# Kernel optimization log

Hardware: AMD Instinct MI355X
Metric: run time of the kernel (lower is better)

## Reference

```python
import jax, jax.numpy as jnp
import numpy as np

N = 262144
BN_EPS = 1e-5


def gcn_conv(x, edge_index, edge_weight, W, b):
    """PyG GCNConv: symmetric norm with added self-loops (fill value 1).
    out[i] = sum_e d^{-1/2}[src] * w_e * d^{-1/2}[dst] * (x[src] @ W) + b
    """
    src, dst = edge_index[0], edge_index[1]
    loops = jnp.arange(N)
    src2 = jnp.concatenate([src, loops])
    dst2 = jnp.concatenate([dst, loops])
    ew2 = jnp.concatenate([edge_weight, jnp.ones((N,), edge_weight.dtype)])
    deg = jax.ops.segment_sum(ew2, dst2, num_segments=N)  # [N]
    dinv = jnp.where(deg > 0, jax.lax.rsqrt(deg), 0.0)
    norm = dinv[src2] * ew2 * dinv[dst2]  # [E+N]
    h = x @ W  # [N, out_c] tiny GEMM
    msg = h[src2] * norm[:, None]  # gather + scale, [E+N, out_c]
    out = jax.ops.segment_sum(msg, dst2, num_segments=N)  # scatter-add
    return out + b


def bn_eval(x, gamma, beta, mean, var):
    # BatchNorm1d in eval mode (running statistics)
    return (x - mean) * (gamma * jax.lax.rsqrt(var + BN_EPS)) + beta


def setup_inputs() -> dict:
    key = jax.random.key(0)
    ks = jax.random.split(key, 16)
    E = 4194304
    inp = {
        "x": jax.random.normal(ks[0], (N, 1), jnp.float32),
        "edge_index": jax.random.randint(ks[1], (2, E), 0, N, jnp.int64),
        "edge_weight": jax.random.uniform(ks[2], (E,), jnp.float32),
        # GCNConv weights (lin has no bias fused; bias added after aggregation)
        "W1": jax.random.normal(ks[3], (1, 16), jnp.float32) * 0.5,
        "b1": jnp.zeros((16,), jnp.float32),
        "W2": jax.random.normal(ks[4], (16, 4), jnp.float32) * 0.25,
        "b2": jnp.zeros((4,), jnp.float32),
        "W3": jax.random.normal(ks[5], (4, 1), jnp.float32) * 0.5,
        "b3": jnp.zeros((1,), jnp.float32),
        # BatchNorm params (eval-mode running stats)
        "g1": jnp.ones((16,), jnp.float32), "be1": jnp.zeros((16,), jnp.float32),
        "m1": jax.random.normal(ks[6], (16,), jnp.float32) * 0.1,
        "v1": jax.random.uniform(ks[7], (16,), jnp.float32, 0.5, 1.5),
        "g2": jnp.ones((4,), jnp.float32), "be2": jnp.zeros((4,), jnp.float32),
        "m2": jax.random.normal(ks[8], (4,), jnp.float32) * 0.1,
        "v2": jax.random.uniform(ks[9], (4,), jnp.float32, 0.5, 1.5),
        # final Linear
        "We": jax.random.normal(ks[10], (1, 1), jnp.float32),
        "bee": jnp.zeros((1,), jnp.float32),
    }
    return inp


def reference(x, edge_index, edge_weight, W1, b1, W2, b2, W3, b3,
              g1, be1, m1, v1, g2, be2, m2, v2, We, bee):
    h = gcn_conv(x, edge_index, edge_weight, W1, b1)
    h = jax.nn.relu(bn_eval(h, g1, be1, m1, v1))  # dropout = identity (eval)
    h = gcn_conv(h, edge_index, edge_weight, W2, b2)
    h = jax.nn.relu(bn_eval(h, g2, be2, m2, v2))
    h = gcn_conv(h, edge_index, edge_weight, W3, b3)
    h = h @ We + bee
    return jax.nn.sigmoid(h)
```

## Files before the change

kernel.cpp:

```cpp
#include <hip/hip_runtime.h>
#include <hip/hip_fp16.h>
#include <math.h>


#define BN_EPS 1e-5f
#define BKT_BITS 9
#define BKT_SZ 512
#define NBKT 512
#define PB 1024
#define PT 512
#define STAGE_CAP 4096
#define CAPR 8960
#define CHUNK_R 9
#define NGRP 128
#define NBL 2048
#define CAP2 2560
#define SW(p) ((p) ^ (((p) >> 5) & 31))

typedef int v2i __attribute__((ext_vector_type(2)));
typedef int v4i __attribute__((ext_vector_type(4)));

__device__ inline int2 ntload2(const int2* p) {
    v2i v = __builtin_nontemporal_load((const v2i*)p);
    return make_int2(v.x, v.y);
}
__device__ inline int4 ntload4(const int4* p) {
    v4i v = __builtin_nontemporal_load((const v4i*)p);
    return make_int4(v.x, v.y, v.z, v.w);
}
__device__ inline int ntloadi(const int* p) { return __builtin_nontemporal_load(p); }
__device__ inline void ntstore2(int2* p, int2 v) {
    v2i t; t.x = v.x; t.y = v.y;
    __builtin_nontemporal_store(t, (v2i*)p);
}
__device__ inline float wdec(int e) {
    return __half2float(__ushort_as_half((unsigned short)((((unsigned)e) >> 18) << 1)));
}

__global__ void k_zero(int* __restrict__ gcur, int m) {
    int i = blockIdx.x * blockDim.x + threadIdx.x;
    if (i < m) gcur[i] = 0;
}

__device__ inline void scat1(int d, int s, int wbits, int* __restrict__ cur,
                             const int* __restrict__ basem, int2* __restrict__ stage) {
    int bk = ((unsigned)d) >> BKT_BITS;
    int dloc = d & (BKT_SZ - 1);
    int pos = atomicAdd(&cur[bk], 1);
    int dest = basem[bk] + pos;
    unsigned h = (unsigned)(__half_as_ushort(__float2half(__int_as_float(wbits))) & 0x7FFF);
    unsigned w14 = (h >> 1) + (h & 1);
    stage[pos] = make_int2(
        (int)((unsigned)s | ((unsigned)dloc << 18) | (((unsigned)dest & 31u) << 27)),
        (int)(w14 | (((unsigned)dest >> 5) << 14)));
}

__global__ __launch_bounds__(PT, 8) void k_scatter(
        const int* __restrict__ src, const int* __restrict__ dst,
        const float* __restrict__ w, int* __restrict__ gcur,
        int2* __restrict__ sorted, int E) {
    __shared__ int cur[NBKT];
    __shared__ int basem[NBKT];
    __shared__ int wsum[8];
    __shared__ int2 stage[STAGE_CAP];
    int t = threadIdx.x, b = blockIdx.x;
    cur[t] = 0;
    __syncthreads();
    int lo = b * STAGE_CAP;
    const int4* dp = (const int4*)(dst + lo);
    int4 d4a = ntload4(dp + t);
    int4 d4b = ntload4(dp + t + PT);
    atomicAdd(&cur[((unsigned)d4a.x) >> BKT_BITS], 1);
    atomicAdd(&cur[((unsigned)d4a.y) >> BKT_BITS], 1);
    atomicAdd(&cur[((unsigned)d4a.z) >> BKT_BITS], 1);
    atomicAdd(&cur[((unsigned)d4a.w) >> BKT_BITS], 1);
    atomicAdd(&cur[((unsigned)d4b.x) >> BKT_BITS], 1);
    atomicAdd(&cur[((unsigned)d4b.y) >> BKT_BITS], 1);
    atomicAdd(&cur[((unsigned)d4b.z) >> BKT_BITS], 1);
    atomicAdd(&cur[((unsigned)d4b.w) >> BKT_BITS], 1);
    __syncthreads();
    int v = cur[t];
    int lane = t & 63, wid = t >> 6;
    int inc = v;
#pragma unroll
    for (int off = 1; off < 64; off <<= 1) {
        int u = __shfl_up(inc, off);
        if (lane >= off) inc += u;
    }
    if (lane == 63) wsum[wid] = inc;
    __syncthreads();
    if (t == 0) {
        int s = 0;
#pragma unroll
        for (int i = 0; i < 8; ++i) { int c = wsum[i]; wsum[i] = s; s += c; }
    }
    __syncthreads();
    int excl = inc - v + wsum[wid];
    int gbase = v ? atomicAdd(&gcur[t << 4], v) : 0;
    cur[t] = excl;
    basem[t] = t * CAPR + gbase - excl;
    __syncthreads();
    const int4* sp = (const int4*)(src + lo);
    const int4* wp = (const int4*)(w + lo);
    int4 s4a = ntload4(sp + t), s4b = ntload4(sp + t + PT);
    int4 w4a = ntload4(wp + t), w4b = ntload4(wp + t + PT);
    scat1(d4a.x, s4a.x, w4a.x, cur, basem, stage);
    scat1(d4a.y, s4a.y, w4a.y, cur, basem, stage);
    scat1(d4a.z, s4a.z, w4a.z, cur, basem, stage);
    scat1(d4a.w, s4a.w, w4a.w, cur, basem, stage);
    scat1(d4b.x, s4b.x, w4b.x, cur, basem, stage);
    scat1(d4b.y, s4b.y, w4b.y, cur, basem, stage);
    scat1(d4b.z, s4b.z, w4b.z, cur, basem, stage);
    scat1(d4b.w, s4b.w, w4b.w, cur, basem, stage);
    __syncthreads();
    for (int p = t; p < STAGE_CAP; p += PT) {
        int2 sv = stage[p];
        unsigned w0 = (unsigned)sv.x, w1 = (unsigned)sv.y;
        int dest = (int)(((w1 >> 14) << 5) | (w0 >> 27));
        ntstore2(&sorted[dest], make_int2((int)(w0 & 0x07FFFFFF), (int)(w1 & 0x3FFF)));
    }
}

__global__ __launch_bounds__(1024, 8) void k_sortdeg(
        const int* __restrict__ gcur, int2* __restrict__ sorted,
        const float* __restrict__ x, float* __restrict__ dinv,
        float* __restrict__ xs, int* __restrict__ starts,
        int* __restrict__ gend) {
    __shared__ int lpk[CAPR];
    __shared__ int cnt[BKT_SZ];
    __shared__ int sts[BKT_SZ + 1];
    int t = threadIdx.x, b = blockIdx.x;
    int lo2 = b * CAPR;
    int len = min(gcur[b << 4], CAPR);
    if (t < BKT_SZ) cnt[t] = 0;
    __syncthreads();

    int e27[CHUNK_R], wrk[CHUNK_R];
#pragma unroll
    for (int r = 0; r < CHUNK_R; ++r) {
        int k = t + (r << 10);
        if (k < len) {
            int2 v = ntload2(&sorted[lo2 + k]);
            e27[r] = v.x;
            int rk = atomicAdd(&cnt[((unsigned)v.x) >> 18], 1);
            wrk[r] = (v.y & 0x3FFF) | (rk << 14);
        }
    }
    __syncthreads();
    int c_own = (t < BKT_SZ) ? cnt[t] : 0;
    for (int o = 1; o < BKT_SZ; o <<= 1) {
        int a = (t < BKT_SZ && t >= o) ? cnt[t - o] : 0;
        __syncthreads();
        if (t < BKT_SZ) cnt[t] += a;
        __syncthreads();
    }
    if (t < BKT_SZ) sts[t] = cnt[t] - c_own;
    if (t == 0) sts[BKT_SZ] = len;
    __syncthreads();
#pragma unroll
    for (int r = 0; r < CHUNK_R; ++r) {
        int k = t + (r << 10);
        if (k < len) {
            int e = e27[r];
            int pos = sts[((unsigned)e) >> 18] + (((unsigned)wrk[r]) >> 14);
            lpk[SW(pos)] = (e & 0x3FFFF) | ((wrk[r] & 0x3FFF) << 18);
        }
    }
    __syncthreads();

    int pbase = 2 * lo2;
    if (t < BKT_SZ) {
        int c0 = sts[t], c1 = sts[t + 1];
        float s = 0.f;
        for (int k = c0; k < c1; ++k) s += wdec(lpk[SW(k)]);
        float di = rsqrtf(1.0f + s);
        int i = b * BKT_SZ + t;
        dinv[i] = di;
        xs[i] = di * x[i];
        starts[i] = pbase + c0;
    }
    if (t < 4)
        gend[b * 4 + t] = pbase + ((t == 3) ? len : sts[(t + 1) * NGRP]);

    int* srtp = (int*)sorted;
    for (int k = t; k < len; k += 1024)
        srtp[pbase + k] = lpk[SW(k)];
}

__global__ __launch_bounds__(512, 8) void k_l1(
        const int* __restrict__ starts, const int* __restrict__ gend,
        const int* __restrict__ srtp,
        const float* __restrict__ xs, const float* __restrict__ dinv,
        const float* __restrict__ W1, const float* __restrict__ b1,
        const float* __restrict__ g1, const float* __restrict__ be1,
        const float* __restrict__ m1, const float* __restrict__ v1,
        const float* __restrict__ W2, int2* __restrict__ hs2p) {
    __shared__ int eds[CAP2];
    __shared__ float part[3][NGRP];
    int t = threadIdx.x, b = blockIdx.x;
    int i0 = b * NGRP;
    int lo = starts[i0];
    int len = min(gend[b] - lo, CAP2);
    for (int k = t; k < len; k += 512) eds[SW(k)] = ntloadi(srtp + lo + k);
    __syncthreads();
    int li = t & (NGRP - 1);
    int j = t >> 7;
    int i = i0 + li;
    int c0 = starts[i] - lo;
    int c1 = (li == NGRP - 1) ? len : starts[i + 1] - lo;
    int seg = c1 - c0;
    int kb = c0 + ((seg * j) >> 2);
    int ke = c0 + ((seg * (j + 1)) >> 2);
    float acc = 0.f;
    for (int k = kb; k < ke; ++k) {
        int e = eds[SW(k)];
        acc = fmaf(wdec(e), xs[e & 0x3FFFF], acc);
    }
    if (j) part[j - 1][li] = acc;
    __syncthreads();
    if (j) return;
    float di = dinv[i];
    float a = di * (acc + part[0][li] + part[1][li] + part[2][li] + xs[i]);
    float h0 = 0.f, h1 = 0.f, h2 = 0.f, h3 = 0.f;
#pragma unroll
    for (int c = 0; c < 16; ++c) {
        float s1c = g1[c] * rsqrtf(v1[c] + BN_EPS);
        float z = fmaf(a, W1[c] * s1c, fmaf(b1[c] - m1[c], s1c, be1[c]));
        z = fmaxf(z, 0.f);
        h0 = fmaf(z, W2[c * 4 + 0], h0);
        h1 = fmaf(z, W2[c * 4 + 1], h1);
        h2 = fmaf(z, W2[c * 4 + 2], h2);
        h3 = fmaf(z, W2[c * 4 + 3], h3);
    }
    __half2 p01 = __floats2half2_rn(di * h0, di * h1);
    __half2 p23 = __floats2half2_rn(di * h2, di * h3);
    hs2p[i] = make_int2(*(int*)&p01, *(int*)&p23);
}

__global__ __launch_bounds__(512, 8) void k_l2(
        const int* __restrict__ starts, const int* __restrict__ gend,
        const int* __restrict__ srtp,
        const int2* __restrict__ hs2p, const float* __restrict__ dinv,
        const float* __restrict__ b2, const float* __restrict__ g2,
        const float* __restrict__ be2, const float* __restrict__ m2,
        const float* __restrict__ v2, const float* __restrict__ W3,
        float* __restrict__ hs3) {
    __shared__ int eds[CAP2];
    __shared__ float4 part4[3][NGRP];
    int t = threadIdx.x, b = blockIdx.x;
    int i0 = b * NGRP;
    int lo = starts[i0];
    int len = min(gend[b] - lo, CAP2);
    for (int k = t; k < len; k += 512) eds[SW(k)] = ntloadi(srtp + lo + k);
    __syncthreads();
    int li = t & (NGRP - 1);
    int j = t >> 7;
    int i = i0 + li;
    int c0 = starts[i] - lo;
    int c1 = (li == NGRP - 1) ? len : starts[i + 1] - lo;
    int seg = c1 - c0;
    int kb = c0 + ((seg * j) >> 2);
    int ke = c0 + ((seg * (j + 1)) >> 2);
    float a0 = 0.f, a1 = 0.f, a2 = 0.f, a3 = 0.f;
    for (int k = kb; k < ke; ++k) {
        int e = eds[SW(k)];
        int2 h = hs2p[e & 0x3FFFF];
        float wv = wdec(e);
        float2 f01 = __half22float2(*(__half2*)&h.x);
        float2 f23 = __half22float2(*(__half2*)&h.y);
        a0 = fmaf(wv, f01.x, a0); a1 = fmaf(wv, f01.y, a1);
        a2 = fmaf(wv, f23.x, a2); a3 = fmaf(wv, f23.y, a3);
    }
    if (j) part4[j - 1][li] = make_float4(a0, a1, a2, a3);
    __syncthreads();
    if (j) return;
    float4 pa = part4[0][li], pb = part4[1][li], pc = part4[2][li];
    float di = dinv[i];
    int2 sp = hs2p[i];
    float2 f01 = __half22float2(*(__half2*)&sp.x);
    float2 f23 = __half22float2(*(__half2*)&sp.y);
    float av[4] = {di * (a0 + pa.x + pb.x + pc.x + f01.x),
                   di * (a1 + pa.y + pb.y + pc.y + f01.y),
                   di * (a2 + pa.z + pb.z + pc.z + f23.x),
                   di * (a3 + pa.w + pb.w + pc.w + f23.y)};
    float h = 0.f;
#pragma unroll
    for (int d = 0; d < 4; ++d) {
        float s2 = g2[d] * rsqrtf(v2[d] + BN_EPS);
        float z = fmaf(av[d] + b2[d] - m2[d], s2, be2[d]);
        z = fmaxf(z, 0.f);
        h = fmaf(z, W3[d], h);
    }
    hs3[i] = di * h;
}

__global__ __launch_bounds__(512, 8) void k_l3(
        const int* __restrict__ starts, const int* __restrict__ gend,
        const int* __restrict__ srtp,
        const float* __restrict__ hs3, const float* __restrict__ dinv,
        const float* __restrict__ b3, const float* __restrict__ We,
        const float* __restrict__ bee, float* __restrict__ out) {
    __shared__ int eds[CAP2];
    __shared__ float part[3][NGRP];
    int t = threadIdx.x, b = blockIdx.x;
    int i0 = b * NGRP;
    int lo = starts[i0];
    int len = min(gend[b] - lo, CAP2);
    for (int k = t; k < len; k += 512) eds[SW(k)] = ntloadi(srtp + lo + k);
    __syncthreads();
    int li = t & (NGRP - 1);
    int j = t >> 7;
    int i = i0 + li;
    int c0 = starts[i] - lo;
    int c1 = (li == NGRP - 1) ? len : starts[i + 1] - lo;
    int seg = c1 - c0;
    int kb = c0 + ((seg * j) >> 2);
    int ke = c0 + ((seg * (j + 1)) >> 2);
    float acc = 0.f;
    for (int k = kb; k < ke; ++k) {
        int e = eds[SW(k)];
        acc = fmaf(wdec(e), hs3[e & 0x3FFFF], acc);
    }
    if (j) part[j - 1][li] = acc;
    __syncthreads();
    if (j) return;
    float a = dinv[i] * (acc + part[0][li] + part[1][li] + part[2][li] + hs3[i]);
    float o = fmaf(a + b3[0], We[0], bee[0]);
    out[i] = 1.0f / (1.0f + expf(-o));
}

extern "C" void kernel_launch(void* const* d_in, const int* in_sizes, int n_in,
                              void* d_out, int out_size, void* d_ws, size_t ws_size,
                              hipStream_t stream) {
    const float* x   = (const float*)d_in[0];
    const int*   ei  = (const int*)d_in[1];
    const float* w   = (const float*)d_in[2];
    const float* W1  = (const float*)d_in[3];
    const float* b1  = (const float*)d_in[4];
    const float* W2  = (const float*)d_in[5];
    const float* b2  = (const float*)d_in[6];
    const float* W3  = (const float*)d_in[7];
    const float* b3  = (const float*)d_in[8];
    const float* g1  = (const float*)d_in[9];
    const float* be1 = (const float*)d_in[10];
    const float* m1  = (const float*)d_in[11];
    const float* v1  = (const float*)d_in[12];
    const float* g2  = (const float*)d_in[13];
    const float* be2 = (const float*)d_in[14];
    const float* m2  = (const float*)d_in[15];
    const float* v2  = (const float*)d_in[16];
    const float* We  = (const float*)d_in[17];
    const float* bee = (const float*)d_in[18];
    float* out = (float*)d_out;

    const int n = in_sizes[0];
    const int E = in_sizes[2];
    const int* src = ei;
    const int* dst = ei + E;

    char* ws = (char*)d_ws;
    int2*  sorted  = (int2*)ws;
    int*   gcur    = (int*)(ws + (size_t)NBKT * CAPR * 8);
    int2*  hs2p    = (int2*)(gcur + NBKT * 16);
    float* dinv    = (float*)(hs2p + n);
    float* xs      = dinv + n;
    float* hs3     = xs + n;
    int*   starts  = (int*)(hs3 + n);
    int*   gend    = starts + n;

    int* srtp = (int*)sorted;

    k_zero<<<(NBKT * 16 + 255) / 256, 256, 0, stream>>>(gcur, NBKT * 16);
    k_scatter<<<PB, PT, 0, stream>>>(src, dst, w, gcur, sorted, E);
    k_sortdeg<<<NBKT, 1024, 0, stream>>>(gcur, sorted, x, dinv, xs, starts, gend);
    k_l1<<<NBL, 512, 0, stream>>>(starts, gend, srtp, xs, dinv,
                                  W1, b1, g1, be1, m1, v1, W2, hs2p);
    k_l2<<<NBL, 512, 0, stream>>>(starts, gend, srtp, hs2p, dinv,
                                  b2, g2, be2, m2, v2, W3, hs3);
    k_l3<<<NBL, 512, 0, stream>>>(starts, gend, srtp, hs3, dinv, b3, We, bee, out);
}
```

Baseline: 259.0 us.

## Replace per-node CSR sort with sharded buckets and LDS atomic aggregation

Drops the second-level per-node sort (k_sortdeg) and the starts/gend CSR arrays. Edges stay bucketed by 512-node range, with each bucket split into 8 shards chosen by block index to spread the global atomic counters. Degree and each layer's aggregation now accumulate through shared-memory float atomics over the bucket's edges, using one 1024-thread block per bucket. This removes a full sort pass and the extra write of sorted data, but adds LDS atomic contention, cuts the block count from 2048 to 512, makes float summation order nondeterministic, and replaces nontemporal loads and stores with plain ones.

Result: slower. 302.9 us (+17.0%).

```diff
diff --git a/kernel.cpp b/kernel.cpp
--- a/kernel.cpp
+++ b/kernel.cpp
@@ -10,31 +10,12 @@
 #define PB 1024
 #define PT 512
 #define STAGE_CAP 4096
-#define CAPR 8960
-#define CHUNK_R 9
-#define NGRP 128
-#define NBL 2048
-#define CAP2 2560
-#define SW(p) ((p) ^ (((p) >> 5) & 31))
-
-typedef int v2i __attribute__((ext_vector_type(2)));
-typedef int v4i __attribute__((ext_vector_type(4)));
-
-__device__ inline int2 ntload2(const int2* p) {
-    v2i v = __builtin_nontemporal_load((const v2i*)p);
-    return make_int2(v.x, v.y);
-}
-__device__ inline int4 ntload4(const int4* p) {
-    v4i v = __builtin_nontemporal_load((const v4i*)p);
-    return make_int4(v.x, v.y, v.z, v.w);
-}
-__device__ inline int ntloadi(const int* p) { return __builtin_nontemporal_load(p); }
-__device__ inline void ntstore2(int2* p, int2 v) {
-    v2i t; t.x = v.x; t.y = v.y;
-    __builtin_nontemporal_store(t, (v2i*)p);
-}
-__device__ inline float wdec(int e) {
-    return __half2float(__ushort_as_half((unsigned short)((((unsigned)e) >> 18) << 1)));
+#define SHD 8
+#define CAPS 1280
+#define CAPR (SHD*CAPS)
+
+__device__ inline float wdec14(int y) {
+    return __half2float(__ushort_as_half((unsigned short)(((unsigned)y) << 1)));
 }
 
 __global__ void k_zero(int* __restrict__ gcur, int m) {
@@ -68,8 +49,12 @@
     __syncthreads();
     int lo = b * STAGE_CAP;
     const int4* dp = (const int4*)(dst + lo);
-    int4 d4a = ntload4(dp + t);
-    int4 d4b = ntload4(dp + t + PT);
+    const int4* sp = (const int4*)(src + lo);
+    const int4* wp = (const int4*)(w + lo);
+    int4 d4a = dp[t];
+    int4 d4b = dp[t + PT];
+    int4 s4a = sp[t], s4b = sp[t + PT];
+    int4 w4a = wp[t], w4b = wp[t + PT];
     atomicAdd(&cur[((unsigned)d4a.x) >> BKT_BITS], 1);
     atomicAdd(&cur[((unsigned)d4a.y) >> BKT_BITS], 1);
     atomicAdd(&cur[((unsigned)d4a.z) >> BKT_BITS], 1);
@@ -96,14 +81,11 @@
     }
     __syncthreads();
     int excl = inc - v + wsum[wid];
-    int gbase = v ? atomicAdd(&gcur[t << 4], v) : 0;
+    int shard = b & (SHD - 1);
+    int gbase = v ? atomicAdd(&gcur[((t << 3) | shard) << 4], v) : 0;
     cur[t] = excl;
-    basem[t] = t * CAPR + gbase - excl;
-    __syncthreads();
-    const int4* sp = (const int4*)(src + lo);
-    const int4* wp = (const int4*)(w + lo);
-    int4 s4a = ntload4(sp + t), s4b = ntload4(sp + t + PT);
-    int4 w4a = ntload4(wp + t), w4b = ntload4(wp + t + PT);
+    basem[t] = t * CAPR + shard * CAPS + gbase - excl;
+    __syncthreads();
     scat1(d4a.x, s4a.x, w4a.x, cur, basem, stage);
     scat1(d4a.y, s4a.y, w4a.y, cur, basem, stage);
     scat1(d4a.z, s4a.z, w4a.z, cur, basem, stage);
@@ -117,115 +99,73 @@
         int2 sv = stage[p];
         unsigned w0 = (unsigned)sv.x, w1 = (unsigned)sv.y;
         int dest = (int)(((w1 >> 14) << 5) | (w0 >> 27));
-        ntstore2(&sorted[dest], make_int2((int)(w0 & 0x07FFFFFF), (int)(w1 & 0x3FFF)));
-    }
-}
-
-__global__ __launch_bounds__(1024, 8) void k_sortdeg(
-        const int* __restrict__ gcur, int2* __restrict__ sorted,
+        sorted[dest] = make_int2((int)(w0 & 0x07FFFFFF), (int)(w1 & 0x3FFF));
+    }
+}
+
+__global__ __launch_bounds__(1024, 8) void k_deg(
+        const int* __restrict__ gcur, const int2* __restrict__ sorted,
         const float* __restrict__ x, float* __restrict__ dinv,
-        float* __restrict__ xs, int* __restrict__ starts,
-        int* __restrict__ gend) {
-    __shared__ int lpk[CAPR];
-    __shared__ int cnt[BKT_SZ];
-    __shared__ int sts[BKT_SZ + 1];
-    int t = threadIdx.x, b = blockIdx.x;
-    int lo2 = b * CAPR;
-    int len = min(gcur[b << 4], CAPR);
-    if (t < BKT_SZ) cnt[t] = 0;
-    __syncthreads();
-
-    int e27[CHUNK_R], wrk[CHUNK_R];
-#pragma unroll
-    for (int r = 0; r < CHUNK_R; ++r) {
-        int k = t + (r << 10);
-        if (k < len) {
-            int2 v = ntload2(&sorted[lo2 + k]);
-            e27[r] = v.x;
-            int rk = atomicAdd(&cnt[((unsigned)v.x) >> 18], 1);
-            wrk[r] = (v.y & 0x3FFF) | (rk << 14);
+        float* __restrict__ xs) {
+    __shared__ float accw[BKT_SZ];
+    int t = threadIdx.x, b = blockIdx.x;
+    if (t < BKT_SZ) accw[t] = 0.f;
+    __syncthreads();
+#pragma unroll 1
+    for (int s = 0; s < SHD; ++s) {
+        int c = min(gcur[((b << 3) | s) << 4], CAPS);
+        const int2* p = sorted + b * CAPR + s * CAPS;
+        for (int k = t; k < c; k += 1024) {
+            int2 v = p[k];
+            atomicAdd(&accw[((unsigned)v.x) >> 18], wdec14(v.y));
         }
     }
     __syncthreads();
-    int c_own = (t < BKT_SZ) ? cnt[t] : 0;
-    for (int o = 1; o < BKT_SZ; o <<= 1) {
-        int a = (t < BKT_SZ && t >= o) ? cnt[t - o] : 0;
-        __syncthreads();
-        if (t < BKT_SZ) cnt[t] += a;
-        __syncthreads();
-    }
-    if (t < BKT_SZ) sts[t] = cnt[t] - c_own;
-    if (t == 0) sts[BKT_SZ] = len;
-    __syncthreads();
-#pragma unroll
-    for (int r = 0; r < CHUNK_R; ++r) {
-        int k = t + (r << 10);
-        if (k < len) {
-            int e = e27[r];
-            int pos = sts[((unsigned)e) >> 18] + (((unsigned)wrk[r]) >> 14);
-            lpk[SW(pos)] = (e & 0x3FFFF) | ((wrk[r] & 0x3FFF) << 18);
-        }
-    }
-    __syncthreads();
-
-    int pbase = 2 * lo2;
     if (t < BKT_SZ) {
-        int c0 = sts[t], c1 = sts[t + 1];
-        float s = 0.f;
-        for (int k = c0; k < c1; ++k) s += wdec(lpk[SW(k)]);
-        float di = rsqrtf(1.0f + s);
         int i = b * BKT_SZ + t;
+        float di = rsqrtf(1.0f + accw[t]);
         dinv[i] = di;
         xs[i] = di * x[i];
-        starts[i] = pbase + c0;
-    }
-    if (t < 4)
-        gend[b * 4 + t] = pbase + ((t == 3) ? len : sts[(t + 1) * NGRP]);
-
-    int* srtp = (int*)sorted;
-    for (int k = t; k < len; k += 1024)
-        srtp[pbase + k] = lpk[SW(k)];
-}
-
-__global__ __launch_bounds__(512, 8) void k_l1(
-        const int* __restrict__ starts, const int* __restrict__ gend,
-        const int* __restrict__ srtp,
+    }
+}
+
+__global__ __launch_bounds__(1024, 8) void k_l1(
+        const int* __restrict__ gcur, const int2* __restrict__ sorted,
         const float* __restrict__ xs, const float* __restrict__ dinv,
         const float* __restrict__ W1, const float* __restrict__ b1,
         const float* __restrict__ g1, const float* __restrict__ be1,
         const float* __restrict__ m1, const float* __restrict__ v1,
         const float* __restrict__ W2, int2* __restrict__ hs2p) {
-    __shared__ int eds[CAP2];
-    __shared__ float part[3][NGRP];
-    int t = threadIdx.x, b = blockIdx.x;
-    int i0 = b * NGRP;
-    int lo = starts[i0];
-    int len = min(gend[b] - lo, CAP2);
-    for (int k = t; k < len; k += 512) eds[SW(k)] = ntloadi(srtp + lo + k);
-    __syncthreads();
-    int li = t & (NGRP - 1);
-    int j = t >> 7;
-    int i = i0 + li;
-    int c0 = starts[i] - lo;
-    int c1 = (li == NGRP - 1) ? len : starts[i + 1] - lo;
-    int seg = c1 - c0;
-    int kb = c0 + ((seg * j) >> 2);
-    int ke = c0 + ((seg * (j + 1)) >> 2);
-    float acc = 0.f;
-    for (int k = kb; k < ke; ++k) {
-        int e = eds[SW(k)];
-        acc = fmaf(wdec(e), xs[e & 0x3FFFF], acc);
-    }
-    if (j) part[j - 1][li] = acc;
-    __syncthreads();
-    if (j) return;
+    __shared__ float acc[BKT_SZ];
+    __shared__ float s1w[16], bb1[16];
+    int t = threadIdx.x, b = blockIdx.x;
+    if (t < BKT_SZ) acc[t] = 0.f;
+    if (t >= BKT_SZ && t < BKT_SZ + 16) {
+        int c = t - BKT_SZ;
+        float s = g1[c] * rsqrtf(v1[c] + BN_EPS);
+        s1w[c] = W1[c] * s;
+        bb1[c] = fmaf(b1[c] - m1[c], s, be1[c]);
+    }
+    __syncthreads();
+#pragma unroll 1
+    for (int s = 0; s < SHD; ++s) {
+        int c = min(gcur[((b << 3) | s) << 4], CAPS);
+        const int2* p = sorted + b * CAPR + s * CAPS;
+        for (int k = t; k < c; k += 1024) {
+            int2 v = p[k];
+            atomicAdd(&acc[((unsigned)v.x) >> 18],
+                      wdec14(v.y) * xs[v.x & 0x3FFFF]);
+        }
+    }
+    __syncthreads();
+    if (t >= BKT_SZ) return;
+    int i = b * BKT_SZ + t;
     float di = dinv[i];
-    float a = di * (acc + part[0][li] + part[1][li] + part[2][li] + xs[i]);
+    float a = di * (acc[t] + xs[i]);
     float h0 = 0.f, h1 = 0.f, h2 = 0.f, h3 = 0.f;
 #pragma unroll
     for (int c = 0; c < 16; ++c) {
-        float s1c = g1[c] * rsqrtf(v1[c] + BN_EPS);
-        float z = fmaf(a, W1[c] * s1c, fmaf(b1[c] - m1[c], s1c, be1[c]));
+        float z = fmaf(a, s1w[c], bb1[c]);
         z = fmaxf(z, 0.f);
         h0 = fmaf(z, W2[c * 4 + 0], h0);
         h1 = fmaf(z, W2[c * 4 + 1], h1);
@@ -237,94 +177,86 @@
     hs2p[i] = make_int2(*(int*)&p01, *(int*)&p23);
 }
 
-__global__ __launch_bounds__(512, 8) void k_l2(
-        const int* __restrict__ starts, const int* __restrict__ gend,
-        const int* __restrict__ srtp,
+__global__ __launch_bounds__(1024, 8) void k_l2(
+        const int* __restrict__ gcur, const int2* __restrict__ sorted,
         const int2* __restrict__ hs2p, const float* __restrict__ dinv,
         const float* __restrict__ b2, const float* __restrict__ g2,
         const float* __restrict__ be2, const float* __restrict__ m2,
         const float* __restrict__ v2, const float* __restrict__ W3,
         float* __restrict__ hs3) {
-    __shared__ int eds[CAP2];
-    __shared__ float4 part4[3][NGRP];
-    int t = threadIdx.x, b = blockIdx.x;
-    int i0 = b * NGRP;
-    int lo = starts[i0];
-    int len = min(gend[b] - lo, CAP2);
-    for (int k = t; k < len; k += 512) eds[SW(k)] = ntloadi(srtp + lo + k);
-    __syncthreads();
-    int li = t & (NGRP - 1);
-    int j = t >> 7;
-    int i = i0 + li;
-    int c0 = starts[i] - lo;
-    int c1 = (li == NGRP - 1) ? len : starts[i + 1] - lo;
-    int seg = c1 - c0;
-    int kb = c0 + ((seg * j) >> 2);
-    int ke = c0 + ((seg * (j + 1)) >> 2);
-    float a0 = 0.f, a1 = 0.f, a2 = 0.f, a3 = 0.f;
-    for (int k = kb; k < ke; ++k) {
-        int e = eds[SW(k)];
-        int2 h = hs2p[e & 0x3FFFF];
-        float wv = wdec(e);
-        float2 f01 = __half22float2(*(__half2*)&h.x);
-        float2 f23 = __half22float2(*(__half2*)&h.y);
-        a0 = fmaf(wv, f01.x, a0); a1 = fmaf(wv, f01.y, a1);
-        a2 = fmaf(wv, f23.x, a2); a3 = fmaf(wv, f23.y, a3);
-    }
-    if (j) part4[j - 1][li] = make_float4(a0, a1, a2, a3);
-    __syncthreads();
-    if (j) return;
-    float4 pa = part4[0][li], pb = part4[1][li], pc = part4[2][li];
+    __shared__ float acc4[4][BKT_SZ];
+    __shared__ float s2w[4], bb2[4];
+    int t = threadIdx.x, b = blockIdx.x;
+    if (t < BKT_SZ) {
+        acc4[0][t] = 0.f; acc4[1][t] = 0.f;
+        acc4[2][t] = 0.f; acc4[3][t] = 0.f;
+    }
+    if (t >= BKT_SZ && t < BKT_SZ + 4) {
+        int d = t - BKT_SZ;
+        float s = g2[d] * rsqrtf(v2[d] + BN_EPS);
+        s2w[d] = s;
+        bb2[d] = fmaf(b2[d] - m2[d], s, be2[d]);
+    }
+    __syncthreads();
+#pragma unroll 1
+    for (int s = 0; s < SHD; ++s) {
+        int c = min(gcur[((b << 3) | s) << 4], CAPS);
+        const int2* p = sorted + b * CAPR + s * CAPS;
+        for (int k = t; k < c; k += 1024) {
+            int2 v = p[k];
+            int dl = ((unsigned)v.x) >> 18;
+            int2 h = hs2p[v.x & 0x3FFFF];
+            float wv = wdec14(v.y);
+            float2 f01 = __half22float2(*(__half2*)&h.x);
+            float2 f23 = __half22float2(*(__half2*)&h.y);
+            atomicAdd(&acc4[0][dl], wv * f01.x);
+            atomicAdd(&acc4[1][dl], wv * f01.y);
+            atomicAdd(&acc4[2][dl], wv * f23.x);
+            atomicAdd(&acc4[3][dl], wv * f23.y);
+        }
+    }
+    __syncthreads();
+    if (t >= BKT_SZ) return;
+    int i = b * BKT_SZ + t;
     float di = dinv[i];
     int2 sp = hs2p[i];
     float2 f01 = __half22float2(*(__half2*)&sp.x);
     float2 f23 = __half22float2(*(__half2*)&sp.y);
-    float av[4] = {di * (a0 + pa.x + pb.x + pc.x + f01.x),
-                   di * (a1 + pa.y + pb.y + pc.y + f01.y),
-                   di * (a2 + pa.z + pb.z + pc.z + f23.x),
-                   di * (a3 + pa.w + pb.w + pc.w + f23.y)};
-    float h = 0.f;
-#pragma unroll
-    for (int d = 0; d < 4; ++d) {
-        float s2 = g2[d] * rsqrtf(v2[d] + BN_EPS);
-        float z = fmaf(av[d] + b2[d] - m2[d], s2, be2[d]);
-        z = fmaxf(z, 0.f);
-        h = fmaf(z, W3[d], h);
-    }
+    float av0 = di * (acc4[0][t] + f01.x);
+    float av1 = di * (acc4[1][t] + f01.y);
+    float av2 = di * (acc4[2][t] + f23.x);
+    float av3 = di * (acc4[3][t] + f23.y);
+    float z0 = fmaxf(fmaf(av0, s2w[0], bb2[0]), 0.f);
+    float z1 = fmaxf(fmaf(av1, s2w[1], bb2[1]), 0.f);
+    float z2 = fmaxf(fmaf(av2, s2w[2], bb2[2]), 0.f);
+    float z3 = fmaxf(fmaf(av3, s2w[3], bb2[3]), 0.f);
+    float h = fmaf(z0, W3[0], fmaf(z1, W3[1], fmaf(z2, W3[2], z3 * W3[3])));
     hs3[i] = di * h;
 }
 
-__global__ __launch_bounds__(512, 8) void k_l3(
-        const int* __restrict__ starts, const int* __restrict__ gend,
-        const int* __restrict__ srtp,
+__global__ __launch_bounds__(1024, 8) void k_l3(
+        const int* __restrict__ gcur, const int2* __restrict__ sorted,
         const float* __restrict__ hs3, const float* __restrict__ dinv,
         const float* __restrict__ b3, const float* __restrict__ We,
         const float* __restrict__ bee, float* __restrict__ out) {
-    __shared__ int eds[CAP2];
-    __shared__ float part[3][NGRP];
-    int t = threadIdx.x, b = blockIdx.x;
-    int i0 = b * NGRP;
-    int lo = starts[i0];
-    int len = min(gend[b] - lo, CAP2);
-    for (int k = t; k < len; k += 512) eds[SW(k)] = ntloadi(srtp + lo + k);
-    __syncthreads();
-    int li = t & (NGRP - 1);
-    int j = t >> 7;
-    int i = i0 + li;
-    int c0 = starts[i] - lo;
-    int c1 = (li == NGRP - 1) ? len : starts[i + 1] - lo;
-    int seg = c1 - c0;
-    int kb = c0 + ((seg * j) >> 2);
-    int ke = c0 + ((seg * (j + 1)) >> 2);
-    float acc = 0.f;
-    for (int k = kb; k < ke; ++k) {
-        int e = eds[SW(k)];
-        acc = fmaf(wdec(e), hs3[e & 0x3FFFF], acc);
-    }
-    if (j) part[j - 1][li] = acc;
-    __syncthreads();
-    if (j) return;
-    float a = dinv[i] * (acc + part[0][li] + part[1][li] + part[2][li] + hs3[i]);
+    __shared__ float acc[BKT_SZ];
+    int t = threadIdx.x, b = blockIdx.x;
+    if (t < BKT_SZ) acc[t] = 0.f;
+    __syncthreads();
+#pragma unroll 1
+    for (int s = 0; s < SHD; ++s) {
+        int c = min(gcur[((b << 3) | s) << 4], CAPS);
+        const int2* p = sorted + b * CAPR + s * CAPS;
+        for (int k = t; k < c; k += 1024) {
+            int2 v = p[k];
+            atomicAdd(&acc[((unsigned)v.x) >> 18],
+                      wdec14(v.y) * hs3[v.x & 0x3FFFF]);
+        }
+    }
+    __syncthreads();
+    if (t >= BKT_SZ) return;
+    int i = b * BKT_SZ + t;
+    float a = dinv[i] * (acc[t] + hs3[i]);
     float o = fmaf(a + b3[0], We[0], bee[0]);
     out[i] = 1.0f / (1.0f + expf(-o));
 }
@@ -361,21 +293,17 @@
     char* ws = (char*)d_ws;
     int2*  sorted  = (int2*)ws;
     int*   gcur    = (int*)(ws + (size_t)NBKT * CAPR * 8);
-    int2*  hs2p    = (int2*)(gcur + NBKT * 16);
+    int2*  hs2p    = (int2*)(gcur + NBKT * SHD * 16);
     float* dinv    = (float*)(hs2p + n);
     float* xs      = dinv + n;
     float* hs3     = xs + n;
-    int*   starts  = (int*)(hs3 + n);
-    int*   gend    = starts + n;
-
-    int* srtp = (int*)sorted;
-
-    k_zero<<<(NBKT * 16 + 255) / 256, 256, 0, stream>>>(gcur, NBKT * 16);
+
+    k_zero<<<(NBKT * SHD * 16 + 255) / 256, 256, 0, stream>>>(gcur, NBKT * SHD * 16);
     k_scatter<<<PB, PT, 0, stream>>>(src, dst, w, gcur, sorted, E);
-    k_sortdeg<<<NBKT, 1024, 0, stream>>>(gcur, sorted, x, dinv, xs, starts, gend);
-    k_l1<<<NBL, 512, 0, stream>>>(starts, gend, srtp, xs, dinv,
-                                  W1, b1, g1, be1, m1, v1, W2, hs2p);
-    k_l2<<<NBL, 512, 0, stream>>>(starts, gend, srtp, hs2p, dinv,
-                                  b2, g2, be2, m2, v2, W3, hs3);
-    k_l3<<<NBL, 512, 0, stream>>>(starts, gend, srtp, hs3, dinv, b3, We, bee, out);
-}
+    k_deg<<<NBKT, 1024, 0, stream>>>(gcur, sorted, x, dinv, xs);
+    k_l1<<<NBKT, 1024, 0, stream>>>(gcur, sorted, xs, dinv,
+                                    W1, b1, g1, be1, m1, v1, W2, hs2p);
+    k_l2<<<NBKT, 1024, 0, stream>>>(gcur, sorted, hs2p, dinv,
+                                    b2, g2, be2, m2, v2, W3, hs3);
+    k_l3<<<NBKT, 1024, 0, stream>>>(gcur, sorted, hs3, dinv, b3, We, bee, out);
+}
```
